# Kernel tuning notes

Hardware: AMD Instinct MI355X
Metric: run time of the kernel (lower is better)

Reference implementation:

```python
import jax, jax.numpy as jnp
import numpy as np

B, NW, H, K = 64, 256, 768, 4
K1, Bp, AVDL = 0.1, 1.2, 50.0
ALPHA = 1.0 / H  # 1 / interaction_rep_size
BETA = 0.1


def setup_inputs() -> dict:
    key = jax.random.key(0)
    k1, k2, k3, k4, k5, k6 = jax.random.split(key, 6)
    return {
        "q_rep": jax.random.normal(k1, (B, NW, H), dtype=jnp.float32),
        "d_rep": jax.random.normal(k2, (B, NW, H), dtype=jnp.float32),
        "qtw": jax.random.uniform(k3, (B, NW), dtype=jnp.float32),
        "q_input_ids": jax.random.randint(k4, (B, NW, K), 0, 32, dtype=jnp.int32),
        "d_input_ids": jax.random.randint(k5, (B, NW, K), 0, 32, dtype=jnp.int32),
        "d_tfs": jax.random.randint(k6, (B, NW), 0, 10, dtype=jnp.int32),
    }


def _null_mask(input_ids):
    # [B, NW, 1] float mask: 0 where the whole window is zero ids
    all_zero = jnp.all(input_ids == 0, axis=2)
    return (~all_zero).astype(jnp.float32)[:, :, None]


def reference(q_rep, d_rep, qtw, q_input_ids, d_input_ids, d_tfs):
    q = q_rep * _null_mask(q_input_ids)
    d = d_rep * _null_mask(d_input_ids)

    # term-overlap scores: [B, NW, NW]
    d_expanded_tf = jnp.einsum("bqh,bdh->bqd", q, d)

    # exact match between q windows and d windows: [B, NW, NW]
    em_f = jnp.all(q_input_ids[:, :, None, :] == d_input_ids[:, None, :, :],
                   axis=3).astype(jnp.float32)

    # blended expanded term frequency, weighted by doc term frequencies
    d_tf = d_expanded_tf * (ALPHA * BETA) + em_f * (1.0 - BETA)
    tf_mult = d_tfs.astype(jnp.float32)[:, None, :]          # [B, 1, NW]
    expanded_term_df = jnp.sum(d_tf * tf_mult, axis=2)       # [B, NW]

    # BM25-like scoring
    dl = jnp.sum(d_tfs.astype(jnp.float32), axis=1, keepdims=True)  # [B, 1]
    denom = expanded_term_df * (1.0 + K1)
    nom = expanded_term_df + K1 * (1.0 - Bp + Bp * dl / AVDL)
    dtw = denom / (nom + 1e-8)
    s = jnp.sum(qtw * dtw, axis=1)                           # [B]
    return s, d_expanded_tf
```

## Files before the change

kernel.cpp:

```cpp
#include <hip/hip_runtime.h>
#include <hip/hip_bf16.h>

#define B_   64
#define NW_  256
#define H_   768

#define AB_    (0.1f / 768.0f)
#define OMB_   0.9f
#define K1_    0.1f
#define BP_    1.2f
#define AVDL_  50.0f

typedef __bf16 bf16x4 __attribute__((ext_vector_type(4)));
typedef __bf16 bf16x8 __attribute__((ext_vector_type(8)));
typedef float  f32x4  __attribute__((ext_vector_type(4)));

#define BAR_LGKM() asm volatile("s_waitcnt lgkmcnt(0)\n\ts_barrier" ::: "memory")

__global__ __launch_bounds__(512, 2) void gemm_fused(
    const float* __restrict__ q_rep, const float* __restrict__ d_rep,
    const int* __restrict__ q_ids, const int* __restrict__ d_ids,
    const int* __restrict__ d_tfs,
    float* __restrict__ S, float* __restrict__ ws_etdf)
{
    __shared__ __align__(16) __bf16 As[2][128][40];
    __shared__ __align__(16) __bf16 Bs[2][64][40];
    __shared__ float mq_s[128];
    __shared__ float md_s[64];
    __shared__ float mdtf_s[64];
    __shared__ float tf_s[64];
    __shared__ int4  qk_s[128];
    __shared__ int4  dk_s[64];

    const int tid  = threadIdx.x;
    const int wave = tid >> 6;
    const int lane = tid & 63;
    const int bid  = blockIdx.x;
    const int b    = bid & 63;
    const int t    = bid >> 6;
    const int m0   = (t & 1) * 128;
    const int n0   = (t >> 1) * 64;

    if (tid < 128) {
        int4 qa = *(const int4*)(q_ids + ((size_t)b * NW_ + m0 + tid) * 4);
        qk_s[tid] = qa;
        mq_s[tid] = (qa.x == 0 && qa.y == 0 && qa.z == 0 && qa.w == 0) ? 0.f : 1.f;
    } else if (tid < 192) {
        const int r = tid - 128;
        int4 da = *(const int4*)(d_ids + ((size_t)b * NW_ + n0 + r) * 4);
        dk_s[r] = da;
        float md = (da.x == 0 && da.y == 0 && da.z == 0 && da.w == 0) ? 0.f : 1.f;
        float tf = (float)d_tfs[(size_t)b * NW_ + n0 + r];
        md_s[r]   = md;
        tf_s[r]   = tf;
        mdtf_s[r] = md * tf;
    }

    const int srow = tid >> 3;
    const int sseg = tid & 7;
    const float* Abase = q_rep + ((size_t)b * NW_ + m0) * H_;
    const float* Bbase = d_rep + ((size_t)b * NW_ + n0) * H_;

    float4 ra0[2], ra1[2];
    float4 rb0, rb1;

    auto loadg = [&](float4 (&ra)[2], float4 &rb, int kc) {
#pragma unroll
        for (int i = 0; i < 2; ++i)
            ra[i] = *(const float4*)(Abase + (size_t)(i * 64 + srow) * H_
                                     + kc * 32 + sseg * 4);
        rb = *(const float4*)(Bbase + (size_t)srow * H_ + kc * 32 + sseg * 4);
    };
    auto stage = [&](float4 (&ra)[2], float4 &rb, int buf) {
#pragma unroll
        for (int i = 0; i < 2; ++i) {
            bf16x4 va = { (__bf16)ra[i].x, (__bf16)ra[i].y,
                          (__bf16)ra[i].z, (__bf16)ra[i].w };
            *(bf16x4*)&As[buf][i * 64 + srow][sseg * 4] = va;
        }
        bf16x4 vb = { (__bf16)rb.x, (__bf16)rb.y, (__bf16)rb.z, (__bf16)rb.w };
        *(bf16x4*)&Bs[buf][srow][sseg * 4] = vb;
    };

    f32x4 acc[2][2];
#pragma unroll
    for (int i = 0; i < 2; ++i)
#pragma unroll
        for (int j = 0; j < 2; ++j)
            acc[i][j] = (f32x4){0.f, 0.f, 0.f, 0.f};

    const int fr = lane & 15;
    const int fk = (lane >> 4) * 8;
    const int qm = wave >> 1;
    const int qn = wave & 1;

    loadg(ra0, rb0, 0);
    loadg(ra1, rb1, 1);
    stage(ra0, rb0, 0);
    BAR_LGKM();

#pragma unroll
    for (int kc = 0; kc < 24; ++kc) {
        const int buf = kc & 1;
        if (kc < 22) {
            if ((kc & 1) == 0) loadg(ra0, rb0, kc + 2);
            else               loadg(ra1, rb1, kc + 2);
        }
        bf16x8 af[2], bfr[2];
#pragma unroll
        for (int t2 = 0; t2 < 2; ++t2) {
            af[t2]  = *(bf16x8*)&As[buf][qm * 32 + t2 * 16 + fr][fk];
            bfr[t2] = *(bf16x8*)&Bs[buf][qn * 32 + t2 * 16 + fr][fk];
        }
#pragma unroll
        for (int i = 0; i < 2; ++i)
#pragma unroll
            for (int j = 0; j < 2; ++j)
                acc[i][j] = __builtin_amdgcn_mfma_f32_16x16x32_bf16(
                    af[i], bfr[j], acc[i][j], 0, 0, 0);
        if (kc < 23) {
            const int nb = buf ^ 1;
            if (((kc + 1) & 1) == 0) stage(ra0, rb0, nb);
            else                     stage(ra1, rb1, nb);
        }
        BAR_LGKM();
    }

    const int cn = lane & 15;
    const int qg = lane >> 4;
    float md_l[2], mdtf_l[2], tf_l[2];
    int4  dk_l[2];
#pragma unroll
    for (int j = 0; j < 2; ++j) {
        const int c = qn * 32 + j * 16 + cn;
        md_l[j]   = md_s[c];
        mdtf_l[j] = mdtf_s[c];
        tf_l[j]   = tf_s[c];
        dk_l[j]   = dk_s[c];
    }
    float* Sbase = S + ((size_t)b * NW_ + m0 + qm * 32) * NW_ + n0 + qn * 32;

    float rs[8];
#pragma unroll
    for (int i = 0; i < 2; ++i)
#pragma unroll
        for (int r = 0; r < 4; ++r) {
            const int row = i * 16 + qg * 4 + r;
            const float mq = mq_s[qm * 32 + row];
            const int4  qk = qk_s[qm * 32 + row];
            float sdot = 0.f, sem = 0.f;
#pragma unroll
            for (int j = 0; j < 2; ++j) {
                const float v = acc[i][j][r];
                __builtin_nontemporal_store(v * mq * md_l[j],
                    &Sbase[(size_t)row * NW_ + j * 16 + cn]);
                sdot += v * mdtf_l[j];
                const int4 dk = dk_l[j];
                if (dk.x == qk.x && dk.y == qk.y && dk.z == qk.z && dk.w == qk.w)
                    sem += tf_l[j];
            }
            rs[i * 4 + r] = mq * AB_ * sdot + OMB_ * sem;
        }
#pragma unroll
    for (int off = 1; off <= 8; off <<= 1)
#pragma unroll
        for (int e = 0; e < 8; ++e)
            rs[e] += __shfl_xor(rs[e], off);
    if (cn == 0) {
#pragma unroll
        for (int i = 0; i < 2; ++i)
#pragma unroll
            for (int r = 0; r < 4; ++r)
                atomicAdd(&ws_etdf[(size_t)b * NW_ + m0 + qm * 32 + i * 16 + qg * 4 + r],
                          rs[i * 4 + r]);
    }
}

__global__ __launch_bounds__(64) void final_kernel(
    const float* __restrict__ ws_etdf, const int* __restrict__ d_tfs,
    const float* __restrict__ qtw, float* __restrict__ out)
{
    const int b = blockIdx.x;
    const int lane = threadIdx.x;

    float4 ev = *(const float4*)(ws_etdf + (size_t)b * NW_ + lane * 4);
    int4  tf4 = *(const int4*)(d_tfs   + (size_t)b * NW_ + lane * 4);
    float4 qv = *(const float4*)(qtw    + (size_t)b * NW_ + lane * 4);

    float dl = (float)(tf4.x + tf4.y + tf4.z + tf4.w);
#pragma unroll
    for (int off = 32; off; off >>= 1) dl += __shfl_xor(dl, off);

    const float c = K1_ * (1.f - BP_ + BP_ * dl / AVDL_);
    float ew[4] = {ev.x, ev.y, ev.z, ev.w};
    float qw[4] = {qv.x, qv.y, qv.z, qv.w};
    float s = 0.f;
#pragma unroll
    for (int j = 0; j < 4; ++j)
        s += qw[j] * (ew[j] * (1.f + K1_)) / (ew[j] + c + 1e-8f);
#pragma unroll
    for (int off = 32; off; off >>= 1) s += __shfl_xor(s, off);
    if (lane == 0) out[b] = s;
}

extern "C" void kernel_launch(void* const* d_in, const int* in_sizes, int n_in,
                              void* d_out, int out_size, void* d_ws, size_t ws_size,
                              hipStream_t stream)
{
    const float* q_rep = (const float*)d_in[0];
    const float* d_rep = (const float*)d_in[1];
    const float* qtw   = (const float*)d_in[2];
    const int*   q_ids = (const int*)d_in[3];
    const int*   d_ids = (const int*)d_in[4];
    const int*   d_tfs = (const int*)d_in[5];

    float* out = (float*)d_out;
    float* S   = out + B_;
    float* ws_etdf = (float*)d_ws;

    hipMemsetAsync(ws_etdf, 0, (size_t)B_ * NW_ * sizeof(float), stream);

    gemm_fused<<<512, 512, 0, stream>>>(q_rep, d_rep, q_ids, d_ids, d_tfs,
                                        S, ws_etdf);
    final_kernel<<<B_, 64, 0, stream>>>(ws_etdf, d_tfs, qtw, out);
}
```

Before: 149.5 us.

## Load MFMA fragments directly from global memory, dropping LDS staging

Removes the double-buffered LDS staging and per-iteration barriers. Each of four waves now loads its bf16 fragments straight from global memory and computes a 32x64 output slice. Blocks shrink to 256 threads. The d_rep tile is now fetched redundantly by every wave, relying on L1/L2 for reuse. The fully unrolled loop is left to the compiler for latency hiding, and the nontemporal hint is dropped from the S stores.

```diff
diff --git a/kernel.cpp b/kernel.cpp
--- a/kernel.cpp
+++ b/kernel.cpp
@@ -11,20 +11,15 @@
 #define BP_    1.2f
 #define AVDL_  50.0f
 
-typedef __bf16 bf16x4 __attribute__((ext_vector_type(4)));
 typedef __bf16 bf16x8 __attribute__((ext_vector_type(8)));
 typedef float  f32x4  __attribute__((ext_vector_type(4)));
 
-#define BAR_LGKM() asm volatile("s_waitcnt lgkmcnt(0)\n\ts_barrier" ::: "memory")
-
-__global__ __launch_bounds__(512, 2) void gemm_fused(
+__global__ __launch_bounds__(256, 2) void gemm_fused(
     const float* __restrict__ q_rep, const float* __restrict__ d_rep,
     const int* __restrict__ q_ids, const int* __restrict__ d_ids,
     const int* __restrict__ d_tfs,
     float* __restrict__ S, float* __restrict__ ws_etdf)
 {
-    __shared__ __align__(16) __bf16 As[2][128][40];
-    __shared__ __align__(16) __bf16 Bs[2][64][40];
     __shared__ float mq_s[128];
     __shared__ float md_s[64];
     __shared__ float mdtf_s[64];
@@ -55,90 +50,68 @@
         tf_s[r]   = tf;
         mdtf_s[r] = md * tf;
     }
+    __syncthreads();
 
-    const int srow = tid >> 3;
-    const int sseg = tid & 7;
-    const float* Abase = q_rep + ((size_t)b * NW_ + m0) * H_;
-    const float* Bbase = d_rep + ((size_t)b * NW_ + n0) * H_;
+    const int fr = lane & 15;
+    const int fk = (lane >> 4) * 8;
 
-    float4 ra0[2], ra1[2];
-    float4 rb0, rb1;
+    const float* A_0 = q_rep + ((size_t)b * NW_ + m0 + wave * 32 + fr) * H_ + fk;
+    const float* A_1 = A_0 + 16 * H_;
+    const float* B_0 = d_rep + ((size_t)b * NW_ + n0 + fr) * H_ + fk;
+    const float* B_1 = B_0 + 16 * H_;
+    const float* B_2 = B_0 + 32 * H_;
+    const float* B_3 = B_0 + 48 * H_;
 
-    auto loadg = [&](float4 (&ra)[2], float4 &rb, int kc) {
-#pragma unroll
-        for (int i = 0; i < 2; ++i)
-            ra[i] = *(const float4*)(Abase + (size_t)(i * 64 + srow) * H_
-                                     + kc * 32 + sseg * 4);
-        rb = *(const float4*)(Bbase + (size_t)srow * H_ + kc * 32 + sseg * 4);
-    };
-    auto stage = [&](float4 (&ra)[2], float4 &rb, int buf) {
-#pragma unroll
-        for (int i = 0; i < 2; ++i) {
-            bf16x4 va = { (__bf16)ra[i].x, (__bf16)ra[i].y,
-                          (__bf16)ra[i].z, (__bf16)ra[i].w };
-            *(bf16x4*)&As[buf][i * 64 + srow][sseg * 4] = va;
-        }
-        bf16x4 vb = { (__bf16)rb.x, (__bf16)rb.y, (__bf16)rb.z, (__bf16)rb.w };
-        *(bf16x4*)&Bs[buf][srow][sseg * 4] = vb;
-    };
-
-    f32x4 acc[2][2];
+    f32x4 acc[2][4];
 #pragma unroll
     for (int i = 0; i < 2; ++i)
 #pragma unroll
-        for (int j = 0; j < 2; ++j)
+        for (int j = 0; j < 4; ++j)
             acc[i][j] = (f32x4){0.f, 0.f, 0.f, 0.f};
-
-    const int fr = lane & 15;
-    const int fk = (lane >> 4) * 8;
-    const int qm = wave >> 1;
-    const int qn = wave & 1;
-
-    loadg(ra0, rb0, 0);
-    loadg(ra1, rb1, 1);
-    stage(ra0, rb0, 0);
-    BAR_LGKM();
 
 #pragma unroll
     for (int kc = 0; kc < 24; ++kc) {
-        const int buf = kc & 1;
-        if (kc < 22) {
-            if ((kc & 1) == 0) loadg(ra0, rb0, kc + 2);
-            else               loadg(ra1, rb1, kc + 2);
-        }
-        bf16x8 af[2], bfr[2];
-#pragma unroll
-        for (int t2 = 0; t2 < 2; ++t2) {
-            af[t2]  = *(bf16x8*)&As[buf][qm * 32 + t2 * 16 + fr][fk];
-            bfr[t2] = *(bf16x8*)&Bs[buf][qn * 32 + t2 * 16 + fr][fk];
-        }
+        float4 a0l = *(const float4*)(A_0 + kc * 32);
+        float4 a0h = *(const float4*)(A_0 + kc * 32 + 4);
+        float4 a1l = *(const float4*)(A_1 + kc * 32);
+        float4 a1h = *(const float4*)(A_1 + kc * 32 + 4);
+        float4 b0l = *(const float4*)(B_0 + kc * 32);
+        float4 b0h = *(const float4*)(B_0 + kc * 32 + 4);
+        float4 b1l = *(const float4*)(B_1 + kc * 32);
+        float4 b1h = *(const float4*)(B_1 + kc * 32 + 4);
+        float4 b2l = *(const float4*)(B_2 + kc * 32);
+        float4 b2h = *(const float4*)(B_2 + kc * 32 + 4);
+        float4 b3l = *(const float4*)(B_3 + kc * 32);
+        float4 b3h = *(const float4*)(B_3 + kc * 32 + 4);
+
+        auto mk = [](const float4& lo, const float4& hi) -> bf16x8 {
+            return (bf16x8){ (__bf16)lo.x, (__bf16)lo.y, (__bf16)lo.z, (__bf16)lo.w,
+                             (__bf16)hi.x, (__bf16)hi.y, (__bf16)hi.z, (__bf16)hi.w };
+        };
+        bf16x8 af[2] = { mk(a0l, a0h), mk(a1l, a1h) };
+        bf16x8 bf[4] = { mk(b0l, b0h), mk(b1l, b1h), mk(b2l, b2h), mk(b3l, b3h) };
+
 #pragma unroll
         for (int i = 0; i < 2; ++i)
 #pragma unroll
-            for (int j = 0; j < 2; ++j)
+            for (int j = 0; j < 4; ++j)
                 acc[i][j] = __builtin_amdgcn_mfma_f32_16x16x32_bf16(
-                    af[i], bfr[j], acc[i][j], 0, 0, 0);
-        if (kc < 23) {
-            const int nb = buf ^ 1;
-            if (((kc + 1) & 1) == 0) stage(ra0, rb0, nb);
-            else                     stage(ra1, rb1, nb);
-        }
-        BAR_LGKM();
+                    af[i], bf[j], acc[i][j], 0, 0, 0);
     }
 
     const int cn = lane & 15;
     const int qg = lane >> 4;
-    float md_l[2], mdtf_l[2], tf_l[2];
-    int4  dk_l[2];
+    float md_l[4], mdtf_l[4], tf_l[4];
+    int4  dk_l[4];
 #pragma unroll
-    for (int j = 0; j < 2; ++j) {
-        const int c = qn * 32 + j * 16 + cn;
+    for (int j = 0; j < 4; ++j) {
+        const int c = j * 16 + cn;
         md_l[j]   = md_s[c];
         mdtf_l[j] = mdtf_s[c];
         tf_l[j]   = tf_s[c];
         dk_l[j]   = dk_s[c];
     }
-    float* Sbase = S + ((size_t)b * NW_ + m0 + qm * 32) * NW_ + n0 + qn * 32;
+    float* Sbase = S + ((size_t)b * NW_ + m0 + wave * 32) * NW_ + n0;
 
     float rs[8];
 #pragma unroll
@@ -146,14 +119,13 @@
 #pragma unroll
         for (int r = 0; r < 4; ++r) {
             const int row = i * 16 + qg * 4 + r;
-            const float mq = mq_s[qm * 32 + row];
-            const int4  qk = qk_s[qm * 32 + row];
+            const float mq = mq_s[wave * 32 + row];
+            const int4  qk = qk_s[wave * 32 + row];
             float sdot = 0.f, sem = 0.f;
 #pragma unroll
-            for (int j = 0; j < 2; ++j) {
+            for (int j = 0; j < 4; ++j) {
                 const float v = acc[i][j][r];
-                __builtin_nontemporal_store(v * mq * md_l[j],
-                    &Sbase[(size_t)row * NW_ + j * 16 + cn]);
+                Sbase[(size_t)row * NW_ + j * 16 + cn] = v * mq * md_l[j];
                 sdot += v * mdtf_l[j];
                 const int4 dk = dk_l[j];
                 if (dk.x == qk.x && dk.y == qk.y && dk.z == qk.z && dk.w == qk.w)
@@ -171,7 +143,7 @@
         for (int i = 0; i < 2; ++i)
 #pragma unroll
             for (int r = 0; r < 4; ++r)
-                atomicAdd(&ws_etdf[(size_t)b * NW_ + m0 + qm * 32 + i * 16 + qg * 4 + r],
+                atomicAdd(&ws_etdf[(size_t)b * NW_ + m0 + wave * 32 + i * 16 + qg * 4 + r],
                           rs[i * 4 + r]);
     }
 }
@@ -220,7 +192,7 @@
 
     hipMemsetAsync(ws_etdf, 0, (size_t)B_ * NW_ * sizeof(float), stream);
 
-    gemm_fused<<<512, 512, 0, stream>>>(q_rep, d_rep, q_ids, d_ids, d_tfs,
+    gemm_fused<<<512, 256, 0, stream>>>(q_rep, d_rep, q_ids, d_ids, d_tfs,
                                         S, ws_etdf);
     final_kernel<<<B_, 64, 0, stream>>>(ws_etdf, d_tfs, qtw, out);
 }
```

Result: slower. 186.0 us (+24.4%).
